# Performance work log

Measured on AMD Instinct MI355X. Metric: run time of the kernel, lower is better.

## Reference

```python
import jax, jax.numpy as jnp
import numpy as np

N_WIRES = 4
DIM = 1 << N_WIRES  # 16
N_PATCH = 14 * 14   # 196


def _random_unitary_16(seed=0):
    # Deterministic surrogate for tq.RandomLayer(n_ops=8): a fixed random
    # real orthogonal 16x16 operator applied to the 4-qubit state.
    rng = np.random.default_rng(seed)
    q, _ = np.linalg.qr(rng.standard_normal((DIM, DIM)))
    return jnp.asarray(q, dtype=jnp.float32)


def _linear_params(rng, fan_in, fan_out):
    bound = 1.0 / np.sqrt(fan_in)
    w = rng.uniform(-bound, bound, size=(fan_out, fan_in)).astype(np.float32)
    b = rng.uniform(-bound, bound, size=(fan_out,)).astype(np.float32)
    return jnp.asarray(w), jnp.asarray(b)


def setup_inputs() -> dict:
    key = jax.random.key(0)
    x = jax.random.normal(key, (8192, 784), dtype=jnp.float32)
    rng = np.random.default_rng(1)
    fc1_w, fc1_b = _linear_params(rng, 784, 120)
    fc2_w, fc2_b = _linear_params(rng, 120, 84)
    fc3_w, fc3_b = _linear_params(rng, 84, 1)
    return {
        "x": x,
        "U": _random_unitary_16(),
        "fc1_w": fc1_w, "fc1_b": fc1_b,
        "fc2_w": fc2_w, "fc2_b": fc2_b,
        "fc3_w": fc3_w, "fc3_b": fc3_b,
    }


def _quantum_filter(x, U):
    # x: [b, 784] -> 2x2 patches in row-major order, per-patch wire data
    # [x[r,c], x[r,c+1], x[r+1,c], x[r+1,c+1]]
    b = x.shape[0]
    xp = x.reshape(b, 14, 2, 14, 2).transpose(0, 1, 3, 2, 4).reshape(b, N_PATCH, N_WIRES)
    # Encoder: RY(theta_w) on wire w starting from |0000> -> product state
    c = jnp.cos(0.5 * xp)  # [b, p, 4]
    s = jnp.sin(0.5 * xp)
    a = jnp.stack([c, s], axis=-1)  # [b, p, 4, 2] per-wire amplitudes
    psi = jnp.einsum("bpi,bpj,bpk,bpl->bpijkl",
                     a[:, :, 0], a[:, :, 1], a[:, :, 2], a[:, :, 3])
    psi = psi.reshape(b, N_PATCH, DIM)  # wire 0 = most significant bit
    # Fixed random layer (16x16 unitary)
    psi = jnp.einsum("ij,bpj->bpi", U, psi)
    # PauliZ expectation per wire: sum_i |psi_i|^2 * (1 - 2*bit_w(i))
    idx = jnp.arange(DIM)
    bits = (idx[:, None] >> (N_WIRES - 1 - jnp.arange(N_WIRES))) & 1  # [16, 4]
    zsign = (1 - 2 * bits).astype(psi.dtype)
    meas = jnp.einsum("bpi,iw->bpw", psi * psi, zsign)  # [b, p, 4]
    return meas.reshape(b, N_PATCH * N_WIRES)  # [b, 784]


def reference(x, U, fc1_w, fc1_b, fc2_w, fc2_b, fc3_w, fc3_b):
    feats = _quantum_filter(x, U)
    h = jax.nn.relu(feats @ fc1_w.T + fc1_b)
    h = jax.nn.relu(h @ fc2_w.T + fc2_b)
    logits = (h @ fc3_w.T + fc3_b)[:, 0]  # [b], matches inputs.squeeze()
    # = P(|1>) = (1 + sin(theta)) / 2 (analytic, shot-noise-free)
    exp_val = 0.5 * (1.0 + jnp.sin(logits))
    p = jax.nn.sigmoid(exp_val)
    return jnp.concatenate([p, 1.0 - p], axis=-1)  # [2*b], matches torch.cat on 1-D
```

## Files before the change

### kernel.cpp

```cpp
#include <hip/hip_runtime.h>
#include <hip/hip_bf16.h>
#include <math.h>


#define BATCH   8192
#define NPATCH  196
#define ROWS    8
#define NITEMS  (ROWS * NPATCH)
#define KPAD    800
#define FLD     808
#define H1LD    132

typedef __attribute__((ext_vector_type(8))) short bfrag;
typedef __attribute__((ext_vector_type(4))) short bfrag4;
typedef __attribute__((ext_vector_type(4))) float f32x4;

#if __has_builtin(__builtin_amdgcn_mfma_f32_16x16x16bf16_1k)
#define USE_X16 1
#else
#define USE_X16 0
#endif

static __device__ __forceinline__ unsigned short f2bf(float f) {
    __hip_bfloat16 h = __float2bfloat16(f);
    return __builtin_bit_cast(unsigned short, h);
}
static __device__ __forceinline__ unsigned int pkbf(float lo, float hi) {
    return ((unsigned int)f2bf(hi) << 16) | (unsigned int)f2bf(lo);
}

__global__ __launch_bounds__(256) void w1prep_kernel(
    const float* __restrict__ w1, unsigned short* __restrict__ w1B)
{
    int t = blockIdx.x * 256 + threadIdx.x;
    if (t >= 128 * KPAD) return;
    int n = t / KPAD;
    int k = t - n * KPAD;
    float v = (n < 120 && k < 784) ? w1[n * 784 + k] : 0.f;
    w1B[t] = f2bf(v);
}

__global__ __launch_bounds__(256, 4) void mega_kernel(
    const float* __restrict__ x, const float* __restrict__ U,
    const unsigned short* __restrict__ w1B,
    const float* __restrict__ b1,
    const float* __restrict__ w2, const float* __restrict__ b2,
    const float* __restrict__ w3, const float* __restrict__ b3,
    float* __restrict__ out)
{
    __shared__ __align__(16) unsigned short featsL[ROWS * FLD];
    __shared__ __align__(16) unsigned char pool[8192];

    unsigned short (*psiL)[64][16] =
        reinterpret_cast<unsigned short (*)[64][16]>(pool);
    float* h1L = reinterpret_cast<float*>(pool);
    float* h2L = reinterpret_cast<float*>(pool + ROWS * H1LD * 4);

    const int tid  = threadIdx.x;
    const int lane = tid & 63;
    const int wv   = tid >> 6;
    const int lrow = lane & 15;
    const int lgrp = lane >> 4;
    const int m0   = blockIdx.x * ROWS;

    if (tid < ROWS * 16)
        featsL[(tid >> 4) * FLD + 784 + (tid & 15)] = 0;

#if USE_X16
    bfrag4 Uf16;
    {
        union { bfrag4 f; unsigned int u[2]; } uu;
        float4 a = *reinterpret_cast<const float4*>(U + lrow * 16 + lgrp * 4);
        uu.u[0] = pkbf(a.x, a.y);
        uu.u[1] = pkbf(a.z, a.w);
        Uf16 = uu.f;
    }
    bfrag4 Zf;
    {
        union { bfrag4 f; unsigned int u[2]; } zz;
        if (lrow < 4) {
            float z[4];
#pragma unroll
            for (int j = 0; j < 4; ++j) {
                int k = 4 * lgrp + j;
                z[j] = ((k >> (3 - lrow)) & 1) ? -1.f : 1.f;
            }
            zz.u[0] = pkbf(z[0], z[1]);
            zz.u[1] = pkbf(z[2], z[3]);
        } else {
            zz.u[0] = zz.u[1] = 0u;
        }
        Zf = zz.f;
    }
#else
    bfrag Uf;
    {
        union { bfrag f; unsigned int u[4]; } uu;
        if (lgrp < 2) {
            float4 a = *reinterpret_cast<const float4*>(U + lrow * 16 + lgrp * 8);
            float4 b = *reinterpret_cast<const float4*>(U + lrow * 16 + lgrp * 8 + 4);
            uu.u[0] = pkbf(a.x, a.y); uu.u[1] = pkbf(a.z, a.w);
            uu.u[2] = pkbf(b.x, b.y); uu.u[3] = pkbf(b.z, b.w);
        } else {
            uu.u[0] = uu.u[1] = uu.u[2] = uu.u[3] = 0u;
        }
        Uf = uu.f;
    }
#endif

    for (int c = wv; c < (NITEMS + 63) / 64; c += 4) {
        int item = c * 64 + lane;
        int it   = item < NITEMS - 1 ? item : NITEMS - 1;
        int r  = it / NPATCH;
        int p  = it - r * NPATCH;
        int pr = p / 14;
        int pc = p - pr * 14;
        const float* xr = x + (size_t)(m0 + r) * 784 + pr * 56 + pc * 2;
        float2 xa = *reinterpret_cast<const float2*>(xr);
        float2 xb = *reinterpret_cast<const float2*>(xr + 28);

        float s0, c0, s1, c1, s2, c2, s3, c3;
        __sincosf(0.5f * xa.x, &s0, &c0);
        __sincosf(0.5f * xa.y, &s1, &c1);
        __sincosf(0.5f * xb.x, &s2, &c2);
        __sincosf(0.5f * xb.y, &s3, &c3);

        float t01[4] = {c0 * c1, c0 * s1, s0 * c1, s0 * s1};
        float t23[4] = {c2 * c3, c2 * s3, s2 * c3, s2 * s3};

        unsigned int pw[8];
#pragma unroll
        for (int q = 0; q < 8; ++q) {
            float plo = t01[(2 * q) >> 2]     * t23[(2 * q) & 3];
            float phv = t01[(2 * q + 1) >> 2] * t23[(2 * q + 1) & 3];
            pw[q] = pkbf(plo, phv);
        }
        *reinterpret_cast<uint4*>(&psiL[wv][lane][0]) =
            make_uint4(pw[0], pw[1], pw[2], pw[3]);
        *reinterpret_cast<uint4*>(&psiL[wv][lane][8]) =
            make_uint4(pw[4], pw[5], pw[6], pw[7]);

#pragma unroll
        for (int sub = 0; sub < 4; ++sub) {
            int item16 = c * 64 + sub * 16 + lrow;
#if USE_X16
            bfrag4 Pf = *reinterpret_cast<const bfrag4*>(
                &psiL[wv][sub * 16 + lrow][lgrp * 4]);
            f32x4 dz = {0.f, 0.f, 0.f, 0.f};
            f32x4 d = __builtin_amdgcn_mfma_f32_16x16x16bf16_1k(
                Uf16, Pf, dz, 0, 0, 0);
            union { bfrag4 f; unsigned int u[2]; } qq;
            qq.u[0] = pkbf(d[0] * d[0], d[1] * d[1]);
            qq.u[1] = pkbf(d[2] * d[2], d[3] * d[3]);
            f32x4 m = __builtin_amdgcn_mfma_f32_16x16x16bf16_1k(
                Zf, qq.f, dz, 0, 0, 0);
            if (lgrp == 0 && item16 < NITEMS) {
                int rr = item16 / NPATCH;
                int pp = item16 - rr * NPATCH;
                uint2 o2;
                o2.x = pkbf(m[0], m[1]);
                o2.y = pkbf(m[2], m[3]);
                *reinterpret_cast<uint2*>(&featsL[rr * FLD + pp * 4]) = o2;
            }
#else
            bfrag Bf = {};
            if (lgrp < 2)
                Bf = *reinterpret_cast<const bfrag*>(
                    &psiL[wv][sub * 16 + lrow][lgrp * 8]);
            f32x4 dz = {0.f, 0.f, 0.f, 0.f};
            f32x4 d = __builtin_amdgcn_mfma_f32_16x16x32_bf16(Uf, Bf, dz, 0, 0, 0);
            float q0 = d[0] * d[0], q1 = d[1] * d[1];
            float q2 = d[2] * d[2], q3 = d[3] * d[3];
            float sAll = (q0 + q1) + (q2 + q3);
            float uu2  = (q0 + q1) - (q2 + q3);
            float vv2  = (q0 - q1) + (q2 - q3);
            float t    = __shfl_xor(sAll, 16);
            float Aa   = sAll + t;
            float Bb   = (lane & 16) ? (t - sAll) : (sAll - t);
            t = __shfl_xor(Aa, 32);
            float mw0 = (lane & 32) ? (t - Aa) : (Aa - t);
            float mw1 = Bb + __shfl_xor(Bb, 32);
            float u16 = uu2 + __shfl_xor(uu2, 16);
            float mw2 = u16 + __shfl_xor(u16, 32);
            float v16 = vv2 + __shfl_xor(vv2, 16);
            float mw3 = v16 + __shfl_xor(v16, 32);
            if (lgrp == 0 && item16 < NITEMS) {
                int rr = item16 / NPATCH;
                int pp = item16 - rr * NPATCH;
                ushort4 o;
                o.x = f2bf(mw0); o.y = f2bf(mw1);
                o.z = f2bf(mw2); o.w = f2bf(mw3);
                *reinterpret_cast<ushort4*>(&featsL[rr * FLD + pp * 4]) = o;
            }
#endif
        }
    }
    __syncthreads();

    {
        const unsigned short* fA = &featsL[(lrow & 7) * FLD + lgrp * 8];
        const unsigned short* bp0 =
            w1B + (size_t)(wv * 32 + lrow) * KPAD + lgrp * 8;
        const unsigned short* bp1 = bp0 + 16 * KPAD;

        f32x4 acc0 = {}, acc1 = {};
        for (int k0 = 0; k0 < KPAD; k0 += 32) {
            bfrag a   = *reinterpret_cast<const bfrag*>(fA + k0);
            bfrag b0  = *reinterpret_cast<const bfrag*>(bp0 + k0);
            bfrag b1f = *reinterpret_cast<const bfrag*>(bp1 + k0);
            acc0 = __builtin_amdgcn_mfma_f32_16x16x32_bf16(a, b0, acc0, 0, 0, 0);
            acc1 = __builtin_amdgcn_mfma_f32_16x16x32_bf16(a, b1f, acc1, 0, 0, 0);
        }
        f32x4 accs[2] = {acc0, acc1};
#pragma unroll
        for (int nj = 0; nj < 2; ++nj) {
            int col = wv * 32 + nj * 16 + lrow;
            if (col < 120) {
                float bias = b1[col];
#pragma unroll
                for (int rr2 = 0; rr2 < 4; ++rr2) {
                    int row = lgrp * 4 + rr2;
                    if (row < ROWS)
                        h1L[row * H1LD + col] =
                            fmaxf(accs[nj][rr2] + bias, 0.f);
                }
            }
        }
    }
    __syncthreads();

    for (int e = tid; e < ROWS * 21; e += 256) {
        int r  = e / 21;
        int nq = e - r * 21;
        int n0 = nq * 4;
        float4 bias = *reinterpret_cast<const float4*>(b2 + n0);
        float accv[4] = {bias.x, bias.y, bias.z, bias.w};
#pragma unroll
        for (int kq = 0; kq < 30; ++kq) {
            float4 a = *reinterpret_cast<const float4*>(&h1L[r * H1LD + kq * 4]);
#pragma unroll
            for (int nn = 0; nn < 4; ++nn) {
                const float4 wvv = *reinterpret_cast<const float4*>(
                    w2 + (size_t)(n0 + nn) * 120 + kq * 4);
                accv[nn] = fmaf(a.x, wvv.x, accv[nn]);
                accv[nn] = fmaf(a.y, wvv.y, accv[nn]);
                accv[nn] = fmaf(a.z, wvv.z, accv[nn]);
                accv[nn] = fmaf(a.w, wvv.w, accv[nn]);
            }
        }
        float4 o;
        o.x = fmaxf(accv[0], 0.f);
        o.y = fmaxf(accv[1], 0.f);
        o.z = fmaxf(accv[2], 0.f);
        o.w = fmaxf(accv[3], 0.f);
        *reinterpret_cast<float4*>(&h2L[r * 84 + n0]) = o;
    }
    __syncthreads();

    if (tid < ROWS) {
        int r = tid;
        float acc = b3[0];
#pragma unroll
        for (int kq = 0; kq < 21; ++kq) {
            float4 a   = *reinterpret_cast<const float4*>(&h2L[r * 84 + kq * 4]);
            float4 wvv = *reinterpret_cast<const float4*>(w3 + kq * 4);
            acc = fmaf(a.x, wvv.x, acc);
            acc = fmaf(a.y, wvv.y, acc);
            acc = fmaf(a.z, wvv.z, acc);
            acc = fmaf(a.w, wvv.w, acc);
        }
        float ev = 0.5f * (1.0f + __sinf(acc));
        float pp = 1.0f / (1.0f + __expf(-ev));
        out[m0 + r]         = pp;
        out[BATCH + m0 + r] = 1.0f - pp;
    }
}

extern "C" void kernel_launch(void* const* d_in, const int* in_sizes, int n_in,
                              void* d_out, int out_size, void* d_ws, size_t ws_size,
                              hipStream_t stream)
{
    (void)in_sizes; (void)n_in; (void)out_size; (void)ws_size;
    const float* x  = (const float*)d_in[0];
    const float* U  = (const float*)d_in[1];
    const float* w1 = (const float*)d_in[2];
    const float* b1 = (const float*)d_in[3];
    const float* w2 = (const float*)d_in[4];
    const float* b2 = (const float*)d_in[5];
    const float* w3 = (const float*)d_in[6];
    const float* b3 = (const float*)d_in[7];
    float* out = (float*)d_out;

    unsigned short* w1B = (unsigned short*)d_ws;

    w1prep_kernel<<<dim3((128 * KPAD + 255) / 256), dim3(256), 0, stream>>>(w1, w1B);
    mega_kernel<<<dim3(BATCH / ROWS), dim3(256), 0, stream>>>(
        x, U, w1B, b1, w2, b2, w3, b3, out);
}
```

Baseline: 136.0 us.

## Split fused kernel into quantum-filter kernel and 16-row MLP tail kernel

Splits the fused per-block kernel into two launches. The first is a fully parallel quantum-filter kernel in which each wave handles one 64-patch chunk and writes bf16 features to a global workspace. The second is a tail kernel that runs the MLP on 16 rows per block, so all 16 MFMA rows are used instead of half. This removes the serialized per-block filter loop and the wasted MFMA rows, at the cost of a global write and read of the feature matrix plus an extra launch. The pad columns 784–799 of the global feature buffer are never zeroed, so stale workspace data could reach the padded GEMM (NaN times zero weight gives NaN).

```diff
diff --git a/kernel.cpp b/kernel.cpp
--- a/kernel.cpp
+++ b/kernel.cpp
@@ -5,11 +5,9 @@
 
 #define BATCH   8192
 #define NPATCH  196
-#define ROWS    8
-#define NITEMS  (ROWS * NPATCH)
 #define KPAD    800
-#define FLD     808
 #define H1LD    132
+#define NCHUNKS ((BATCH * NPATCH) / 64)
 
 typedef __attribute__((ext_vector_type(8))) short bfrag;
 typedef __attribute__((ext_vector_type(4))) short bfrag4;
@@ -40,31 +38,17 @@
     w1B[t] = f2bf(v);
 }
 
-__global__ __launch_bounds__(256, 4) void mega_kernel(
+__global__ __launch_bounds__(256) void qfilter_kernel(
     const float* __restrict__ x, const float* __restrict__ U,
-    const unsigned short* __restrict__ w1B,
-    const float* __restrict__ b1,
-    const float* __restrict__ w2, const float* __restrict__ b2,
-    const float* __restrict__ w3, const float* __restrict__ b3,
-    float* __restrict__ out)
-{
-    __shared__ __align__(16) unsigned short featsL[ROWS * FLD];
-    __shared__ __align__(16) unsigned char pool[8192];
-
-    unsigned short (*psiL)[64][16] =
-        reinterpret_cast<unsigned short (*)[64][16]>(pool);
-    float* h1L = reinterpret_cast<float*>(pool);
-    float* h2L = reinterpret_cast<float*>(pool + ROWS * H1LD * 4);
-
-    const int tid  = threadIdx.x;
-    const int lane = tid & 63;
-    const int wv   = tid >> 6;
+    unsigned short* __restrict__ featsB)
+{
+    __shared__ __align__(16) unsigned short psiL[4][64][16];
+
+    const int lane = threadIdx.x & 63;
+    const int wv   = threadIdx.x >> 6;
     const int lrow = lane & 15;
     const int lgrp = lane >> 4;
-    const int m0   = blockIdx.x * ROWS;
-
-    if (tid < ROWS * 16)
-        featsL[(tid >> 4) * FLD + 784 + (tid & 15)] = 0;
+    const int base = (blockIdx.x * 4 + wv) * 64;
 
 #if USE_X16
     bfrag4 Uf16;
@@ -108,14 +92,13 @@
     }
 #endif
 
-    for (int c = wv; c < (NITEMS + 63) / 64; c += 4) {
-        int item = c * 64 + lane;
-        int it   = item < NITEMS - 1 ? item : NITEMS - 1;
-        int r  = it / NPATCH;
-        int p  = it - r * NPATCH;
+    {
+        int item = base + lane;
+        int b  = item / NPATCH;
+        int p  = item - b * NPATCH;
         int pr = p / 14;
         int pc = p - pr * 14;
-        const float* xr = x + (size_t)(m0 + r) * 784 + pr * 56 + pc * 2;
+        const float* xr = x + (size_t)b * 784 + pr * 56 + pc * 2;
         float2 xa = *reinterpret_cast<const float2*>(xr);
         float2 xb = *reinterpret_cast<const float2*>(xr + 28);
 
@@ -139,66 +122,83 @@
             make_uint4(pw[0], pw[1], pw[2], pw[3]);
         *reinterpret_cast<uint4*>(&psiL[wv][lane][8]) =
             make_uint4(pw[4], pw[5], pw[6], pw[7]);
-
-#pragma unroll
-        for (int sub = 0; sub < 4; ++sub) {
-            int item16 = c * 64 + sub * 16 + lrow;
+    }
+
+#pragma unroll
+    for (int sub = 0; sub < 4; ++sub) {
+        int item16 = base + sub * 16 + lrow;
 #if USE_X16
-            bfrag4 Pf = *reinterpret_cast<const bfrag4*>(
-                &psiL[wv][sub * 16 + lrow][lgrp * 4]);
-            f32x4 dz = {0.f, 0.f, 0.f, 0.f};
-            f32x4 d = __builtin_amdgcn_mfma_f32_16x16x16bf16_1k(
-                Uf16, Pf, dz, 0, 0, 0);
-            union { bfrag4 f; unsigned int u[2]; } qq;
-            qq.u[0] = pkbf(d[0] * d[0], d[1] * d[1]);
-            qq.u[1] = pkbf(d[2] * d[2], d[3] * d[3]);
-            f32x4 m = __builtin_amdgcn_mfma_f32_16x16x16bf16_1k(
-                Zf, qq.f, dz, 0, 0, 0);
-            if (lgrp == 0 && item16 < NITEMS) {
-                int rr = item16 / NPATCH;
-                int pp = item16 - rr * NPATCH;
-                uint2 o2;
-                o2.x = pkbf(m[0], m[1]);
-                o2.y = pkbf(m[2], m[3]);
-                *reinterpret_cast<uint2*>(&featsL[rr * FLD + pp * 4]) = o2;
-            }
+        bfrag4 Pf = *reinterpret_cast<const bfrag4*>(
+            &psiL[wv][sub * 16 + lrow][lgrp * 4]);
+        f32x4 dz = {0.f, 0.f, 0.f, 0.f};
+        f32x4 d = __builtin_amdgcn_mfma_f32_16x16x16bf16_1k(Uf16, Pf, dz, 0, 0, 0);
+        union { bfrag4 f; unsigned int u[2]; } qq;
+        qq.u[0] = pkbf(d[0] * d[0], d[1] * d[1]);
+        qq.u[1] = pkbf(d[2] * d[2], d[3] * d[3]);
+        f32x4 m = __builtin_amdgcn_mfma_f32_16x16x16bf16_1k(Zf, qq.f, dz, 0, 0, 0);
+        if (lgrp == 0) {
+            int b16 = item16 / NPATCH;
+            int p16 = item16 - b16 * NPATCH;
+            uint2 o2;
+            o2.x = pkbf(m[0], m[1]);
+            o2.y = pkbf(m[2], m[3]);
+            *reinterpret_cast<uint2*>(featsB + (size_t)b16 * KPAD + p16 * 4) = o2;
+        }
 #else
-            bfrag Bf = {};
-            if (lgrp < 2)
-                Bf = *reinterpret_cast<const bfrag*>(
-                    &psiL[wv][sub * 16 + lrow][lgrp * 8]);
-            f32x4 dz = {0.f, 0.f, 0.f, 0.f};
-            f32x4 d = __builtin_amdgcn_mfma_f32_16x16x32_bf16(Uf, Bf, dz, 0, 0, 0);
-            float q0 = d[0] * d[0], q1 = d[1] * d[1];
-            float q2 = d[2] * d[2], q3 = d[3] * d[3];
-            float sAll = (q0 + q1) + (q2 + q3);
-            float uu2  = (q0 + q1) - (q2 + q3);
-            float vv2  = (q0 - q1) + (q2 - q3);
-            float t    = __shfl_xor(sAll, 16);
-            float Aa   = sAll + t;
-            float Bb   = (lane & 16) ? (t - sAll) : (sAll - t);
-            t = __shfl_xor(Aa, 32);
-            float mw0 = (lane & 32) ? (t - Aa) : (Aa - t);
-            float mw1 = Bb + __shfl_xor(Bb, 32);
-            float u16 = uu2 + __shfl_xor(uu2, 16);
-            float mw2 = u16 + __shfl_xor(u16, 32);
-            float v16 = vv2 + __shfl_xor(vv2, 16);
-            float mw3 = v16 + __shfl_xor(v16, 32);
-            if (lgrp == 0 && item16 < NITEMS) {
-                int rr = item16 / NPATCH;
-                int pp = item16 - rr * NPATCH;
-                ushort4 o;
-                o.x = f2bf(mw0); o.y = f2bf(mw1);
-                o.z = f2bf(mw2); o.w = f2bf(mw3);
-                *reinterpret_cast<ushort4*>(&featsL[rr * FLD + pp * 4]) = o;
-            }
+        bfrag Bf = {};
+        if (lgrp < 2)
+            Bf = *reinterpret_cast<const bfrag*>(
+                &psiL[wv][sub * 16 + lrow][lgrp * 8]);
+        f32x4 dz = {0.f, 0.f, 0.f, 0.f};
+        f32x4 d = __builtin_amdgcn_mfma_f32_16x16x32_bf16(Uf, Bf, dz, 0, 0, 0);
+        float q0 = d[0] * d[0], q1 = d[1] * d[1];
+        float q2 = d[2] * d[2], q3 = d[3] * d[3];
+        float sAll = (q0 + q1) + (q2 + q3);
+        float uu2  = (q0 + q1) - (q2 + q3);
+        float vv2  = (q0 - q1) + (q2 - q3);
+        float t    = __shfl_xor(sAll, 16);
+        float Aa   = sAll + t;
+        float Bb   = ((threadIdx.x & 16)) ? (t - sAll) : (sAll - t);
+        t = __shfl_xor(Aa, 32);
+        float mw0 = ((threadIdx.x & 32)) ? (t - Aa) : (Aa - t);
+        float mw1 = Bb + __shfl_xor(Bb, 32);
+        float u16 = uu2 + __shfl_xor(uu2, 16);
+        float mw2 = u16 + __shfl_xor(u16, 32);
+        float v16 = vv2 + __shfl_xor(vv2, 16);
+        float mw3 = v16 + __shfl_xor(v16, 32);
+        if (lgrp == 0) {
+            int b16 = item16 / NPATCH;
+            int p16 = item16 - b16 * NPATCH;
+            ushort4 o;
+            o.x = f2bf(mw0); o.y = f2bf(mw1);
+            o.z = f2bf(mw2); o.w = f2bf(mw3);
+            *reinterpret_cast<ushort4*>(featsB + (size_t)b16 * KPAD + p16 * 4) = o;
+        }
 #endif
-        }
-    }
-    __syncthreads();
-
-    {
-        const unsigned short* fA = &featsL[(lrow & 7) * FLD + lgrp * 8];
+    }
+}
+
+__global__ __launch_bounds__(256) void tail_kernel(
+    const unsigned short* __restrict__ featsB,
+    const unsigned short* __restrict__ w1B,
+    const float* __restrict__ b1,
+    const float* __restrict__ w2, const float* __restrict__ b2,
+    const float* __restrict__ w3, const float* __restrict__ b3,
+    float* __restrict__ out)
+{
+    __shared__ __align__(16) float h1L[16 * H1LD];
+    __shared__ __align__(16) float h2L[16 * 84];
+
+    const int tid  = threadIdx.x;
+    const int lane = tid & 63;
+    const int wv   = tid >> 6;
+    const int lrow = lane & 15;
+    const int lgrp = lane >> 4;
+    const int m0   = blockIdx.x * 16;
+
+    {
+        const unsigned short* fA =
+            featsB + (size_t)(m0 + lrow) * KPAD + lgrp * 8;
         const unsigned short* bp0 =
             w1B + (size_t)(wv * 32 + lrow) * KPAD + lgrp * 8;
         const unsigned short* bp1 = bp0 + 16 * KPAD;
@@ -218,18 +218,16 @@
             if (col < 120) {
                 float bias = b1[col];
 #pragma unroll
-                for (int rr2 = 0; rr2 < 4; ++rr2) {
-                    int row = lgrp * 4 + rr2;
-                    if (row < ROWS)
-                        h1L[row * H1LD + col] =
-                            fmaxf(accs[nj][rr2] + bias, 0.f);
+                for (int rr = 0; rr < 4; ++rr) {
+                    int row = lgrp * 4 + rr;
+                    h1L[row * H1LD + col] = fmaxf(accs[nj][rr] + bias, 0.f);
                 }
             }
         }
     }
     __syncthreads();
 
-    for (int e = tid; e < ROWS * 21; e += 256) {
+    for (int e = tid; e < 16 * 21; e += 256) {
         int r  = e / 21;
         int nq = e - r * 21;
         int n0 = nq * 4;
@@ -257,7 +255,7 @@
     }
     __syncthreads();
 
-    if (tid < ROWS) {
+    if (tid < 16) {
         int r = tid;
         float acc = b3[0];
 #pragma unroll
@@ -291,9 +289,11 @@
     const float* b3 = (const float*)d_in[7];
     float* out = (float*)d_out;
 
-    unsigned short* w1B = (unsigned short*)d_ws;
+    unsigned short* w1B    = (unsigned short*)d_ws;
+    unsigned short* featsB = w1B + (size_t)128 * KPAD;
 
     w1prep_kernel<<<dim3((128 * KPAD + 255) / 256), dim3(256), 0, stream>>>(w1, w1B);
-    mega_kernel<<<dim3(BATCH / ROWS), dim3(256), 0, stream>>>(
-        x, U, w1B, b1, w2, b2, w3, b3, out);
-}
+    qfilter_kernel<<<dim3(NCHUNKS / 4), dim3(256), 0, stream>>>(x, U, featsB);
+    tail_kernel<<<dim3(BATCH / 16), dim3(256), 0, stream>>>(
+        featsB, w1B, b1, w2, b2, w3, b3, out);
+}
```

After: 136.5 us. No clear change (+0.4%).
